# Optimization experiments

Hardware: AMD Instinct MI355X
Metric: run time of the kernel (lower is better)

## Reference

```python
import jax, jax.numpy as jnp
import numpy as np

N = 100000   # nodes
E = 220000   # directed edges (each branch)
H = 128      # hidden_dim
OUT = 1      # output_dim
G = 4096     # num graphs in batch
PE = 5       # laplacian eigenvector PE dims
VOCAB = 28   # atom types


def gcn_conv(x, src, dst, W, b, n):
    # PyG GCNConv: x' = D^-1/2 (A + I) D^-1/2 (X W) + b
    h = x @ W
    deg = jax.ops.segment_sum(jnp.ones(src.shape[0], x.dtype), dst, num_segments=n) + 1.0
    dinv = jax.lax.rsqrt(deg)
    coef = dinv[src] * dinv[dst]                                    # [E]
    agg = jax.ops.segment_sum(h[src] * coef[:, None], dst, num_segments=n)
    agg = agg + h * (dinv * dinv)[:, None]                          # self-loop term
    return agg + b


def gcn2(x, edge_index, W1, b1, W2, b2, n):
    # PyG GCN model, num_layers=2: conv -> relu -> conv
    src, dst = edge_index[0], edge_index[1]
    h = jax.nn.relu(gcn_conv(x, src, dst, W1, b1, n))
    return gcn_conv(h, src, dst, W2, b2, n)


def setup_inputs() -> dict:
    key = jax.random.key(0)
    ks = jax.random.split(key, 16)
    s = 0.1
    return {
        "node_tokens": jax.random.randint(ks[0], (N, 1), 0, VOCAB),
        "pe": jax.random.normal(ks[1], (N, PE), jnp.float32),
        "edge_index": jax.random.randint(ks[2], (2, E), 0, N),
        "vr_edge_index": jax.random.randint(ks[3], (2, E), 0, N),
        "batch": jnp.sort(jax.random.randint(ks[4], (N,), 0, G)),
        "embed_table": jax.random.normal(ks[5], (VOCAB, H), jnp.float32) * s,
        "Wt": jax.random.normal(ks[6], (PE, H), jnp.float32) * s,
        "bt": jnp.zeros((H,), jnp.float32),
        "W1": jax.random.normal(ks[7], (H, H), jnp.float32) * s,
        "b1": jnp.zeros((H,), jnp.float32),
        "W2": jax.random.normal(ks[8], (H, OUT), jnp.float32) * s,
        "b2": jnp.zeros((OUT,), jnp.float32),
        "Wv1": jax.random.normal(ks[9], (H, H), jnp.float32) * s,
        "bv1": jnp.zeros((H,), jnp.float32),
        "Wv2": jax.random.normal(ks[10], (H, OUT), jnp.float32) * s,
        "bv2": jnp.zeros((OUT,), jnp.float32),
    }


def reference(node_tokens, pe, edge_index, vr_edge_index, batch, embed_table,
              Wt, bt, W1, b1, W2, b2, Wv1, bv1, Wv2, bv2):
    # embed_x(data.x.long()).squeeze(1) + lin_trans(pe)
    x = embed_table[node_tokens[:, 0]] + (pe @ Wt + bt)             # [N, H]
    x1 = gcn2(x, edge_index, W1, b1, W2, b2, N)                     # [N, OUT]
    xv = gcn2(x, vr_edge_index, Wv1, bv1, Wv2, bv2, N)              # [N, OUT]
    x1 = x1 + xv
    y_hat = jax.ops.segment_sum(x1, batch, num_segments=G)          # [G, OUT]
    y_hat = jnp.squeeze(y_hat, axis=-1)                             # [G]
    return (y_hat, x)
```

## Files before the change

kernel.cpp:

```cpp
#include <hip/hip_runtime.h>

#define NN 100000
#define NE 220000
#define HD 128
#define NG 4096
#define NPE 5
#define NB_SCAN ((NN + 255) / 256)
#define NBX4 ((NN * HD / 4) / 256)
#define NBW 128
#define NBD ((2 * NE + 255) / 256)
#define NBAG ((NN + 63) / 64)
#define LDP 136

typedef unsigned int uint;
typedef unsigned short ushort;
typedef __attribute__((ext_vector_type(8))) short bf16x8;
typedef __attribute__((ext_vector_type(4))) float f32x4;

__device__ __forceinline__ float bf2f(uint u16) {
    return __uint_as_float(u16 << 16);
}
__device__ __forceinline__ ushort f2bf(float f) {
    uint u = __float_as_uint(f);
    u += 0x7fffu + ((u >> 16) & 1u);
    return (ushort)(u >> 16);
}

__global__ void k_front(const int* __restrict__ tok, const float* __restrict__ pe,
                        const float* __restrict__ embed, const float* __restrict__ Wtr,
                        const float* __restrict__ bt,
                        float* __restrict__ x, ushort* __restrict__ xb,
                        const float* __restrict__ W1, const float* __restrict__ Wv1,
                        ushort* __restrict__ Wcat,
                        const int* __restrict__ ei, const int* __restrict__ vei,
                        int* __restrict__ cnt) {
    int b = blockIdx.x;
    if (b < NBX4) {
        int idx = b * 256 + threadIdx.x;
        int n = idx >> 5, q = idx & 31;
        int t = tok[n];
        float4 acc = ((const float4*)(embed + (size_t)t * HD))[q];
        float4 bv = ((const float4*)bt)[q];
        acc.x += bv.x; acc.y += bv.y; acc.z += bv.z; acc.w += bv.w;
        const float* pen = pe + n * NPE;
#pragma unroll
        for (int k = 0; k < NPE; ++k) {
            float p = pen[k];
            float4 wv = ((const float4*)(Wtr + k * HD))[q];
            acc.x += p * wv.x; acc.y += p * wv.y;
            acc.z += p * wv.z; acc.w += p * wv.w;
        }
        ((float4*)x)[idx] = acc;
        uint2 pk;
        pk.x = (uint)f2bf(acc.x) | ((uint)f2bf(acc.y) << 16);
        pk.y = (uint)f2bf(acc.z) | ((uint)f2bf(acc.w) << 16);
        ((uint2*)xb)[idx] = pk;
    } else if (b < NBX4 + NBW) {
        int t = (b - NBX4) * 256 + threadIdx.x;
        int f = t >> 7, k = t & 127;
        const float* W = (f < HD) ? W1 : Wv1;
        Wcat[t] = f2bf(W[k * HD + (f & 127)]);
    } else {
        int t = (b - NBX4 - NBW) * 256 + threadIdx.x;
        if (t < 2 * NE) {
            int br = t >= NE;
            int e = t - br * NE;
            const int* S = br ? vei : ei;
            atomicAdd(&cnt[br * NN + S[NE + e]], 1);
        }
    }
}

__global__ void k_scan1(const int* __restrict__ cnt, int* __restrict__ off,
                        int* __restrict__ bsum, float* __restrict__ dinv) {
    __shared__ int s[256];
    int br = blockIdx.x / NB_SCAN;
    int blk = blockIdx.x % NB_SCAN;
    int tid = threadIdx.x;
    int i = blk * 256 + tid;
    int v = (i < NN) ? cnt[br * NN + i] : 0;
    if (i < NN) dinv[br * NN + i] = rsqrtf((float)v + 1.0f);
    s[tid] = v;
    __syncthreads();
    for (int d = 1; d < 256; d <<= 1) {
        int t = (tid >= d) ? s[tid - d] : 0;
        __syncthreads();
        s[tid] += t;
        __syncthreads();
    }
    if (i < NN) off[br * NN + i] = s[tid] - v;
    if (tid == 255) bsum[br * 512 + blk] = s[255];
}

__global__ void k_scan2(int* __restrict__ bsum) {
    __shared__ int s[512];
    int br = blockIdx.x;
    int tid = threadIdx.x;
    int v = (tid < NB_SCAN) ? bsum[br * 512 + tid] : 0;
    s[tid] = v;
    __syncthreads();
    for (int d = 1; d < 512; d <<= 1) {
        int t = (tid >= d) ? s[tid - d] : 0;
        __syncthreads();
        s[tid] += t;
        __syncthreads();
    }
    if (tid < NB_SCAN) bsum[br * 512 + tid] = s[tid] - v;
}

__global__ void k_scan3(int* __restrict__ off, const int* __restrict__ bsum,
                        int* __restrict__ cur) {
    int br = blockIdx.x / NB_SCAN;
    int blk = blockIdx.x % NB_SCAN;
    int i = blk * 256 + threadIdx.x;
    if (i < NN) {
        int o = off[br * NN + i] + bsum[br * 512 + blk];
        off[br * NN + i] = o;
        cur[br * NN + i] = o;
    }
}

__global__ void k_scatter(const int* __restrict__ ei, const int* __restrict__ vei,
                          const float* __restrict__ dinv, int* __restrict__ cur,
                          int2* __restrict__ ent) {
    int t = blockIdx.x * blockDim.x + threadIdx.x;
    if (t >= 2 * NE) return;
    int br = t >= NE;
    int e = t - br * NE;
    const int* S = br ? vei : ei;
    int s = S[e], d = S[NE + e];
    int pos = atomicAdd(&cur[br * NN + d], 1);
    int2 rec;
    rec.x = s;
    rec.y = __float_as_int(dinv[br * NN + s] * dinv[br * NN + d]);
    ent[br * NE + pos] = rec;
}

__global__ __launch_bounds__(256) void k_agg_gemm(
        const ushort* __restrict__ xb, const ushort* __restrict__ Wcat,
        const float* __restrict__ dinv, const int* __restrict__ off,
        const int* __restrict__ cur, const int2* __restrict__ ent,
        const float* __restrict__ b1, const float* __restrict__ bv1,
        const float* __restrict__ W2, const float* __restrict__ Wv2,
        float* __restrict__ z) {
    __shared__ ushort As[64 * LDP];
    int bi = blockIdx.x;
    int br = bi >= NBAG;
    int n0 = (bi - br * NBAG) * 64;
    int tid = threadIdx.x;

    {
        int hw = tid >> 5;
        int l = tid & 31;
        const int2* en = ent + br * NE;
        for (int nn = 0; nn < 8; ++nn) {
            int nl = hw * 8 + nn;
            int n = n0 + nl;
            uint2 pk = {0u, 0u};
            if (n < NN) {
                float dv = dinv[br * NN + n];
                uint2 u = *(const uint2*)(xb + (size_t)n * HD + l * 4);
                float c = dv * dv;
                float a0 = bf2f(u.x & 0xffffu) * c, a1 = bf2f(u.x >> 16) * c;
                float a2 = bf2f(u.y & 0xffffu) * c, a3 = bf2f(u.y >> 16) * c;
                int p0 = off[br * NN + n], p1 = cur[br * NN + n];
                for (int p = p0; p < p1; p += 4) {
                    int2 e0 = en[p], e1 = en[p + 1], e2 = en[p + 2], e3 = en[p + 3];
                    int s0 = e0.x;
                    int s1 = (p + 1 < p1) ? e1.x : n;
                    int s2 = (p + 2 < p1) ? e2.x : n;
                    int s3 = (p + 3 < p1) ? e3.x : n;
                    float c0 = __int_as_float(e0.y);
                    float c1 = (p + 1 < p1) ? __int_as_float(e1.y) : 0.f;
                    float c2 = (p + 2 < p1) ? __int_as_float(e2.y) : 0.f;
                    float c3 = (p + 3 < p1) ? __int_as_float(e3.y) : 0.f;
                    uint2 v0 = *(const uint2*)(xb + (size_t)s0 * HD + l * 4);
                    uint2 v1 = *(const uint2*)(xb + (size_t)s1 * HD + l * 4);
                    uint2 v2 = *(const uint2*)(xb + (size_t)s2 * HD + l * 4);
                    uint2 v3 = *(const uint2*)(xb + (size_t)s3 * HD + l * 4);
                    a0 += bf2f(v0.x & 0xffffu) * c0; a1 += bf2f(v0.x >> 16) * c0;
                    a2 += bf2f(v0.y & 0xffffu) * c0; a3 += bf2f(v0.y >> 16) * c0;
                    a0 += bf2f(v1.x & 0xffffu) * c1; a1 += bf2f(v1.x >> 16) * c1;
                    a2 += bf2f(v1.y & 0xffffu) * c1; a3 += bf2f(v1.y >> 16) * c1;
                    a0 += bf2f(v2.x & 0xffffu) * c2; a1 += bf2f(v2.x >> 16) * c2;
                    a2 += bf2f(v2.y & 0xffffu) * c2; a3 += bf2f(v2.y >> 16) * c2;
                    a0 += bf2f(v3.x & 0xffffu) * c3; a1 += bf2f(v3.x >> 16) * c3;
                    a2 += bf2f(v3.y & 0xffffu) * c3; a3 += bf2f(v3.y >> 16) * c3;
                }
                pk.x = (uint)f2bf(a0) | ((uint)f2bf(a1) << 16);
                pk.y = (uint)f2bf(a2) | ((uint)f2bf(a3) << 16);
            }
            *(uint2*)&As[nl * LDP + l * 4] = pk;
        }
    }
    __syncthreads();

    int w = tid >> 6, lane = tid & 63;
    int m = lane & 15, quad = lane >> 4;
    const ushort* Wg = Wcat + (size_t)br * 128 * 128;
    f32x4 acc[8] = {};
#pragma unroll
    for (int kc = 0; kc < 4; ++kc) {
        int k0 = kc * 32 + quad * 8;
        bf16x8 xf = *(const bf16x8*)&As[(w * 16 + m) * LDP + k0];
#pragma unroll
        for (int ft = 0; ft < 8; ++ft) {
            bf16x8 wf = *(const bf16x8*)&Wg[(ft * 16 + m) * 128 + k0];
            acc[ft] = __builtin_amdgcn_mfma_f32_16x16x32_bf16(wf, xf, acc[ft], 0, 0, 0);
        }
    }
    const float* bb = br ? bv1 : b1;
    const float* ww = br ? Wv2 : W2;
    float part = 0.f;
#pragma unroll
    for (int ft = 0; ft < 8; ++ft) {
        int f0 = ft * 16 + quad * 4;
        float4 b4 = *(const float4*)&bb[f0];
        float4 w4 = *(const float4*)&ww[f0];
        f32x4 a = acc[ft];
        part += fmaxf(a[0] + b4.x, 0.f) * w4.x + fmaxf(a[1] + b4.y, 0.f) * w4.y
              + fmaxf(a[2] + b4.z, 0.f) * w4.z + fmaxf(a[3] + b4.w, 0.f) * w4.w;
    }
    part += __shfl_xor(part, 16);
    part += __shfl_xor(part, 32);
    int n = n0 + w * 16 + m;
    if (quad == 0 && n < NN) z[br * NN + n] = part;
}

__global__ void k_final2(const float* __restrict__ z, const float* __restrict__ dinv,
                         const int* __restrict__ off, const int* __restrict__ cur,
                         const int2* __restrict__ ent,
                         const float* __restrict__ b2, const float* __restrict__ bv2,
                         const int* __restrict__ batch, float* __restrict__ y) {
    __shared__ float ybuf[256];
    __shared__ int gbase_s;
    int br = blockIdx.x >= NB_SCAN;
    int nb = blockIdx.x - br * NB_SCAN;
    int tid = threadIdx.x;
    ybuf[tid] = 0.f;
    if (tid == 0) gbase_s = batch[nb * 256];
    __syncthreads();
    int gbase = gbase_s;
    int n = nb * 256 + tid;
    if (n < NN) {
        const int2* en = ent + br * NE;
        float dv = dinv[br * NN + n];
        float acc = z[br * NN + n] * dv * dv;
        int p1 = cur[br * NN + n];
        for (int p = off[br * NN + n]; p < p1; p += 4) {
            int2 e0 = en[p], e1 = en[p + 1], e2 = en[p + 2], e3 = en[p + 3];
            int s0 = e0.x;
            int s1 = (p + 1 < p1) ? e1.x : n;
            int s2 = (p + 2 < p1) ? e2.x : n;
            int s3 = (p + 3 < p1) ? e3.x : n;
            float c0 = __int_as_float(e0.y);
            float c1 = (p + 1 < p1) ? __int_as_float(e1.y) : 0.f;
            float c2 = (p + 2 < p1) ? __int_as_float(e2.y) : 0.f;
            float c3 = (p + 3 < p1) ? __int_as_float(e3.y) : 0.f;
            acc += c0 * z[br * NN + s0] + c1 * z[br * NN + s1]
                 + c2 * z[br * NN + s2] + c3 * z[br * NN + s3];
        }
        acc += br ? bv2[0] : b2[0];
        int gi = batch[n] - gbase;
        if (gi < 256) atomicAdd(&ybuf[gi], acc);
        else atomicAdd(&y[batch[n]], acc);
    }
    __syncthreads();
    float v = ybuf[tid];
    if (v != 0.f) atomicAdd(&y[gbase + tid], v);
}

extern "C" void kernel_launch(void* const* d_in, const int* in_sizes, int n_in,
                              void* d_out, int out_size, void* d_ws, size_t ws_size,
                              hipStream_t stream) {
    const int*   tok   = (const int*)d_in[0];
    const float* pe    = (const float*)d_in[1];
    const int*   ei    = (const int*)d_in[2];
    const int*   vei   = (const int*)d_in[3];
    const int*   batch = (const int*)d_in[4];
    const float* embed = (const float*)d_in[5];
    const float* Wtr   = (const float*)d_in[6];
    const float* bt    = (const float*)d_in[7];
    const float* W1    = (const float*)d_in[8];
    const float* b1    = (const float*)d_in[9];
    const float* W2    = (const float*)d_in[10];
    const float* b2    = (const float*)d_in[11];
    const float* Wv1   = (const float*)d_in[12];
    const float* bv1   = (const float*)d_in[13];
    const float* Wv2   = (const float*)d_in[14];
    const float* bv2   = (const float*)d_in[15];

    float* y = (float*)d_out;
    float* x = y + NG;

    char* w = (char*)d_ws;
    ushort* xb   = (ushort*)w;               w += (size_t)NN * HD * 2;
    ushort* Wcat = (ushort*)w;               w += 256 * 128 * 2;
    float*  dinv = (float*)w;                w += 2 * NN * 4;
    float*  z    = (float*)w;                w += 2 * NN * 4;
    int*    cnt  = (int*)w;                  w += 2 * NN * 4;
    int*    off  = (int*)w;                  w += 2 * NN * 4;
    int*    cur  = (int*)w;                  w += 2 * NN * 4;
    int2*   ent  = (int2*)w;                 w += (size_t)(2 * NE + 8) * 8;
    int*    bsum = (int*)w;                  w += 2 * 512 * 4;

    hipMemsetAsync(y, 0, NG * sizeof(float), stream);
    hipMemsetAsync(cnt, 0, 2 * NN * sizeof(int), stream);

    k_front<<<NBX4 + NBW + NBD, 256, 0, stream>>>(tok, pe, embed, Wtr, bt, x, xb,
                                                  W1, Wv1, Wcat, ei, vei, cnt);
    k_scan1<<<2 * NB_SCAN, 256, 0, stream>>>(cnt, off, bsum, dinv);
    k_scan2<<<2, 512, 0, stream>>>(bsum);
    k_scan3<<<2 * NB_SCAN, 256, 0, stream>>>(off, bsum, cur);
    k_scatter<<<(2 * NE + 255) / 256, 256, 0, stream>>>(ei, vei, dinv, cur, ent);
    k_agg_gemm<<<2 * NBAG, 256, 0, stream>>>(xb, Wcat, dinv, off, cur, ent,
                                             b1, bv1, W2, Wv2, z);
    k_final2<<<2 * NB_SCAN, 256, 0, stream>>>(z, dinv, off, cur, ent,
                                              b2, bv2, batch, y);
}
```

Before: 274.6 us.

## Replace three-pass scan with atomic wave-level CSR allocation and shrink agg tiles

The three-kernel prefix scan becomes a single kernel in which each wavefront scans its counts with shuffles and reserves a contiguous range through an atomicAdd on a global allocator. This makes CSR segments non-ordered but still contiguous, and the zeroing of y moves into that kernel, removing two launches and a memset. The aggregation+GEMM kernel now handles 16 nodes per 512-thread block, one node per half-wave, instead of 64 nodes per 256 threads, to raise parallelism and cut per-thread serial gather work. The feature dimension is split across waves with a shared-memory reduction, at the cost of reloading W per block and adding a sync.

```diff
diff --git a/kernel.cpp b/kernel.cpp
--- a/kernel.cpp
+++ b/kernel.cpp
@@ -9,7 +9,7 @@
 #define NBX4 ((NN * HD / 4) / 256)
 #define NBW 128
 #define NBD ((2 * NE + 255) / 256)
-#define NBAG ((NN + 63) / 64)
+#define NBAG16 (NN / 16)
 #define LDP 136
 
 typedef unsigned int uint;
@@ -71,50 +71,32 @@
     }
 }
 
-__global__ void k_scan1(const int* __restrict__ cnt, int* __restrict__ off,
-                        int* __restrict__ bsum, float* __restrict__ dinv) {
-    __shared__ int s[256];
-    int br = blockIdx.x / NB_SCAN;
-    int blk = blockIdx.x % NB_SCAN;
+__global__ void k_alloc(const int* __restrict__ cnt, int* __restrict__ alloc,
+                        float* __restrict__ dinv, int* __restrict__ off,
+                        int* __restrict__ cur, float* __restrict__ y) {
     int tid = threadIdx.x;
+    int gid = blockIdx.x * 256 + tid;
+    if (gid < NG) y[gid] = 0.f;
+    int br = blockIdx.x >= NB_SCAN;
+    int blk = blockIdx.x - br * NB_SCAN;
     int i = blk * 256 + tid;
-    int v = (i < NN) ? cnt[br * NN + i] : 0;
-    if (i < NN) dinv[br * NN + i] = rsqrtf((float)v + 1.0f);
-    s[tid] = v;
-    __syncthreads();
-    for (int d = 1; d < 256; d <<= 1) {
-        int t = (tid >= d) ? s[tid - d] : 0;
-        __syncthreads();
-        s[tid] += t;
-        __syncthreads();
-    }
-    if (i < NN) off[br * NN + i] = s[tid] - v;
-    if (tid == 255) bsum[br * 512 + blk] = s[255];
-}
-
-__global__ void k_scan2(int* __restrict__ bsum) {
-    __shared__ int s[512];
-    int br = blockIdx.x;
-    int tid = threadIdx.x;
-    int v = (tid < NB_SCAN) ? bsum[br * 512 + tid] : 0;
-    s[tid] = v;
-    __syncthreads();
-    for (int d = 1; d < 512; d <<= 1) {
-        int t = (tid >= d) ? s[tid - d] : 0;
-        __syncthreads();
-        s[tid] += t;
-        __syncthreads();
-    }
-    if (tid < NB_SCAN) bsum[br * 512 + tid] = s[tid] - v;
-}
-
-__global__ void k_scan3(int* __restrict__ off, const int* __restrict__ bsum,
-                        int* __restrict__ cur) {
-    int br = blockIdx.x / NB_SCAN;
-    int blk = blockIdx.x % NB_SCAN;
-    int i = blk * 256 + threadIdx.x;
+    int lane = tid & 63;
+    int c = 0;
     if (i < NN) {
-        int o = off[br * NN + i] + bsum[br * 512 + blk];
+        c = cnt[br * NN + i];
+        dinv[br * NN + i] = rsqrtf((float)c + 1.0f);
+    }
+    int x = c;
+#pragma unroll
+    for (int o = 1; o < 64; o <<= 1) {
+        int t = __shfl_up(x, o, 64);
+        if (lane >= o) x += t;
+    }
+    int bs = 0;
+    if (lane == 63) bs = atomicAdd(&alloc[br], x);
+    bs = __shfl(bs, 63, 64);
+    if (i < NN) {
+        int o = bs + x - c;
         off[br * NN + i] = o;
         cur[br * NN + i] = o;
     }
@@ -136,95 +118,89 @@
     ent[br * NE + pos] = rec;
 }
 
-__global__ __launch_bounds__(256) void k_agg_gemm(
+__global__ __launch_bounds__(512) void k_agg_gemm(
         const ushort* __restrict__ xb, const ushort* __restrict__ Wcat,
         const float* __restrict__ dinv, const int* __restrict__ off,
         const int* __restrict__ cur, const int2* __restrict__ ent,
         const float* __restrict__ b1, const float* __restrict__ bv1,
         const float* __restrict__ W2, const float* __restrict__ Wv2,
         float* __restrict__ z) {
-    __shared__ ushort As[64 * LDP];
+    __shared__ ushort As[16 * LDP];
+    __shared__ float red[8][16];
     int bi = blockIdx.x;
-    int br = bi >= NBAG;
-    int n0 = (bi - br * NBAG) * 64;
+    int br = bi >= NBAG16;
+    int n0 = (bi - br * NBAG16) * 16;
     int tid = threadIdx.x;
 
     {
-        int hw = tid >> 5;
+        int h = tid >> 5;
         int l = tid & 31;
+        int n = n0 + h;
         const int2* en = ent + br * NE;
-        for (int nn = 0; nn < 8; ++nn) {
-            int nl = hw * 8 + nn;
-            int n = n0 + nl;
-            uint2 pk = {0u, 0u};
-            if (n < NN) {
-                float dv = dinv[br * NN + n];
-                uint2 u = *(const uint2*)(xb + (size_t)n * HD + l * 4);
-                float c = dv * dv;
-                float a0 = bf2f(u.x & 0xffffu) * c, a1 = bf2f(u.x >> 16) * c;
-                float a2 = bf2f(u.y & 0xffffu) * c, a3 = bf2f(u.y >> 16) * c;
-                int p0 = off[br * NN + n], p1 = cur[br * NN + n];
-                for (int p = p0; p < p1; p += 4) {
-                    int2 e0 = en[p], e1 = en[p + 1], e2 = en[p + 2], e3 = en[p + 3];
-                    int s0 = e0.x;
-                    int s1 = (p + 1 < p1) ? e1.x : n;
-                    int s2 = (p + 2 < p1) ? e2.x : n;
-                    int s3 = (p + 3 < p1) ? e3.x : n;
-                    float c0 = __int_as_float(e0.y);
-                    float c1 = (p + 1 < p1) ? __int_as_float(e1.y) : 0.f;
-                    float c2 = (p + 2 < p1) ? __int_as_float(e2.y) : 0.f;
-                    float c3 = (p + 3 < p1) ? __int_as_float(e3.y) : 0.f;
-                    uint2 v0 = *(const uint2*)(xb + (size_t)s0 * HD + l * 4);
-                    uint2 v1 = *(const uint2*)(xb + (size_t)s1 * HD + l * 4);
-                    uint2 v2 = *(const uint2*)(xb + (size_t)s2 * HD + l * 4);
-                    uint2 v3 = *(const uint2*)(xb + (size_t)s3 * HD + l * 4);
-                    a0 += bf2f(v0.x & 0xffffu) * c0; a1 += bf2f(v0.x >> 16) * c0;
-                    a2 += bf2f(v0.y & 0xffffu) * c0; a3 += bf2f(v0.y >> 16) * c0;
-                    a0 += bf2f(v1.x & 0xffffu) * c1; a1 += bf2f(v1.x >> 16) * c1;
-                    a2 += bf2f(v1.y & 0xffffu) * c1; a3 += bf2f(v1.y >> 16) * c1;
-                    a0 += bf2f(v2.x & 0xffffu) * c2; a1 += bf2f(v2.x >> 16) * c2;
-                    a2 += bf2f(v2.y & 0xffffu) * c2; a3 += bf2f(v2.y >> 16) * c2;
-                    a0 += bf2f(v3.x & 0xffffu) * c3; a1 += bf2f(v3.x >> 16) * c3;
-                    a2 += bf2f(v3.y & 0xffffu) * c3; a3 += bf2f(v3.y >> 16) * c3;
-                }
-                pk.x = (uint)f2bf(a0) | ((uint)f2bf(a1) << 16);
-                pk.y = (uint)f2bf(a2) | ((uint)f2bf(a3) << 16);
-            }
-            *(uint2*)&As[nl * LDP + l * 4] = pk;
-        }
+        float dv = dinv[br * NN + n];
+        uint2 u = *(const uint2*)(xb + (size_t)n * HD + l * 4);
+        float c = dv * dv;
+        float a0 = bf2f(u.x & 0xffffu) * c, a1 = bf2f(u.x >> 16) * c;
+        float a2 = bf2f(u.y & 0xffffu) * c, a3 = bf2f(u.y >> 16) * c;
+        int p0 = off[br * NN + n], p1 = cur[br * NN + n];
+        for (int p = p0; p < p1; p += 4) {
+            int2 e0 = en[p], e1 = en[p + 1], e2 = en[p + 2], e3 = en[p + 3];
+            int s0 = e0.x;
+            int s1 = (p + 1 < p1) ? e1.x : n;
+            int s2 = (p + 2 < p1) ? e2.x : n;
+            int s3 = (p + 3 < p1) ? e3.x : n;
+            float c0 = __int_as_float(e0.y);
+            float c1 = (p + 1 < p1) ? __int_as_float(e1.y) : 0.f;
+            float c2 = (p + 2 < p1) ? __int_as_float(e2.y) : 0.f;
+            float c3 = (p + 3 < p1) ? __int_as_float(e3.y) : 0.f;
+            uint2 v0 = *(const uint2*)(xb + (size_t)s0 * HD + l * 4);
+            uint2 v1 = *(const uint2*)(xb + (size_t)s1 * HD + l * 4);
+            uint2 v2 = *(const uint2*)(xb + (size_t)s2 * HD + l * 4);
+            uint2 v3 = *(const uint2*)(xb + (size_t)s3 * HD + l * 4);
+            a0 += bf2f(v0.x & 0xffffu) * c0; a1 += bf2f(v0.x >> 16) * c0;
+            a2 += bf2f(v0.y & 0xffffu) * c0; a3 += bf2f(v0.y >> 16) * c0;
+            a0 += bf2f(v1.x & 0xffffu) * c1; a1 += bf2f(v1.x >> 16) * c1;
+            a2 += bf2f(v1.y & 0xffffu) * c1; a3 += bf2f(v1.y >> 16) * c1;
+            a0 += bf2f(v2.x & 0xffffu) * c2; a1 += bf2f(v2.x >> 16) * c2;
+            a2 += bf2f(v2.y & 0xffffu) * c2; a3 += bf2f(v2.y >> 16) * c2;
+            a0 += bf2f(v3.x & 0xffffu) * c3; a1 += bf2f(v3.x >> 16) * c3;
+            a2 += bf2f(v3.y & 0xffffu) * c3; a3 += bf2f(v3.y >> 16) * c3;
+        }
+        uint2 pk;
+        pk.x = (uint)f2bf(a0) | ((uint)f2bf(a1) << 16);
+        pk.y = (uint)f2bf(a2) | ((uint)f2bf(a3) << 16);
+        *(uint2*)&As[h * LDP + l * 4] = pk;
     }
     __syncthreads();
 
     int w = tid >> 6, lane = tid & 63;
     int m = lane & 15, quad = lane >> 4;
     const ushort* Wg = Wcat + (size_t)br * 128 * 128;
-    f32x4 acc[8] = {};
+    f32x4 acc = {};
 #pragma unroll
     for (int kc = 0; kc < 4; ++kc) {
         int k0 = kc * 32 + quad * 8;
-        bf16x8 xf = *(const bf16x8*)&As[(w * 16 + m) * LDP + k0];
-#pragma unroll
-        for (int ft = 0; ft < 8; ++ft) {
-            bf16x8 wf = *(const bf16x8*)&Wg[(ft * 16 + m) * 128 + k0];
-            acc[ft] = __builtin_amdgcn_mfma_f32_16x16x32_bf16(wf, xf, acc[ft], 0, 0, 0);
-        }
+        bf16x8 xf = *(const bf16x8*)&As[m * LDP + k0];
+        bf16x8 wf = *(const bf16x8*)&Wg[(w * 16 + m) * 128 + k0];
+        acc = __builtin_amdgcn_mfma_f32_16x16x32_bf16(wf, xf, acc, 0, 0, 0);
     }
     const float* bb = br ? bv1 : b1;
     const float* ww = br ? Wv2 : W2;
-    float part = 0.f;
-#pragma unroll
-    for (int ft = 0; ft < 8; ++ft) {
-        int f0 = ft * 16 + quad * 4;
-        float4 b4 = *(const float4*)&bb[f0];
-        float4 w4 = *(const float4*)&ww[f0];
-        f32x4 a = acc[ft];
-        part += fmaxf(a[0] + b4.x, 0.f) * w4.x + fmaxf(a[1] + b4.y, 0.f) * w4.y
-              + fmaxf(a[2] + b4.z, 0.f) * w4.z + fmaxf(a[3] + b4.w, 0.f) * w4.w;
-    }
+    int f0 = w * 16 + quad * 4;
+    float4 b4 = *(const float4*)&bb[f0];
+    float4 w4 = *(const float4*)&ww[f0];
+    float part = fmaxf(acc[0] + b4.x, 0.f) * w4.x + fmaxf(acc[1] + b4.y, 0.f) * w4.y
+               + fmaxf(acc[2] + b4.z, 0.f) * w4.z + fmaxf(acc[3] + b4.w, 0.f) * w4.w;
     part += __shfl_xor(part, 16);
     part += __shfl_xor(part, 32);
-    int n = n0 + w * 16 + m;
-    if (quad == 0 && n < NN) z[br * NN + n] = part;
+    if (lane < 16) red[w][lane] = part;
+    __syncthreads();
+    if (tid < 16) {
+        float s = 0.f;
+#pragma unroll
+        for (int i = 0; i < 8; ++i) s += red[i][tid];
+        z[br * NN + n0 + tid] = s;
+    }
 }
 
 __global__ void k_final2(const float* __restrict__ z, const float* __restrict__ dinv,
@@ -298,23 +274,20 @@
     ushort* Wcat = (ushort*)w;               w += 256 * 128 * 2;
     float*  dinv = (float*)w;                w += 2 * NN * 4;
     float*  z    = (float*)w;                w += 2 * NN * 4;
-    int*    cnt  = (int*)w;                  w += 2 * NN * 4;
+    int*    cnt  = (int*)w;                  w += (2 * NN + 2) * 4;
     int*    off  = (int*)w;                  w += 2 * NN * 4;
     int*    cur  = (int*)w;                  w += 2 * NN * 4;
     int2*   ent  = (int2*)w;                 w += (size_t)(2 * NE + 8) * 8;
-    int*    bsum = (int*)w;                  w += 2 * 512 * 4;
-
-    hipMemsetAsync(y, 0, NG * sizeof(float), stream);
-    hipMemsetAsync(cnt, 0, 2 * NN * sizeof(int), stream);
+    int*    alloc = cnt + 2 * NN;
+
+    hipMemsetAsync(cnt, 0, (2 * NN + 2) * sizeof(int), stream);
 
     k_front<<<NBX4 + NBW + NBD, 256, 0, stream>>>(tok, pe, embed, Wtr, bt, x, xb,
                                                   W1, Wv1, Wcat, ei, vei, cnt);
-    k_scan1<<<2 * NB_SCAN, 256, 0, stream>>>(cnt, off, bsum, dinv);
-    k_scan2<<<2, 512, 0, stream>>>(bsum);
-    k_scan3<<<2 * NB_SCAN, 256, 0, stream>>>(off, bsum, cur);
+    k_alloc<<<2 * NB_SCAN, 256, 0, stream>>>(cnt, alloc, dinv, off, cur, y);
     k_scatter<<<(2 * NE + 255) / 256, 256, 0, stream>>>(ei, vei, dinv, cur, ent);
-    k_agg_gemm<<<2 * NBAG, 256, 0, stream>>>(xb, Wcat, dinv, off, cur, ent,
-                                             b1, bv1, W2, Wv2, z);
+    k_agg_gemm<<<2 * NBAG16, 512, 0, stream>>>(xb, Wcat, dinv, off, cur, ent,
+                                               b1, bv1, W2, Wv2, z);
     k_final2<<<2 * NB_SCAN, 256, 0, stream>>>(z, dinv, off, cur, ent,
                                               b2, bv2, batch, y);
 }
```

Result: slower. 289.0 us (+5.2%).

## Parallelize aggregation over edges with LDS fp32 atomics and 512-thread blocks

Applied to the files above, without the earlier changes.

The aggregation in the fused agg+GEMM kernel now distributes the edge range of each 64-node tile across 16 half-waves instead of assigning 8 nodes per half-wave. Partial sums accumulate in a swizzled fp32 LDS tile through shared-memory atomics, which requires storing the destination node in each CSR entry (int2 widened to int4). The GEMM is remapped so each of 8 waves owns 16 output features across all 64 nodes, followed by a cross-wave reduction. The y memset is folded into the scan kernel. This targets load imbalance from skewed degrees, at the cost of doubled entry bandwidth, LDS atomic contention and 32KB+ of LDS per block.

```diff
diff --git a/kernel.cpp b/kernel.cpp
--- a/kernel.cpp
+++ b/kernel.cpp
@@ -9,7 +9,7 @@
 #define NBX4 ((NN * HD / 4) / 256)
 #define NBW 128
 #define NBD ((2 * NE + 255) / 256)
-#define NBAG ((NN + 63) / 64)
+#define NBT ((NN + 63) / 64)
 #define LDP 136
 
 typedef unsigned int uint;
@@ -72,11 +72,14 @@
 }
 
 __global__ void k_scan1(const int* __restrict__ cnt, int* __restrict__ off,
-                        int* __restrict__ bsum, float* __restrict__ dinv) {
+                        int* __restrict__ bsum, float* __restrict__ dinv,
+                        float* __restrict__ y) {
     __shared__ int s[256];
+    int tid = threadIdx.x;
+    int gid = blockIdx.x * 256 + tid;
+    if (gid < NG) y[gid] = 0.f;
     int br = blockIdx.x / NB_SCAN;
     int blk = blockIdx.x % NB_SCAN;
-    int tid = threadIdx.x;
     int i = blk * 256 + tid;
     int v = (i < NN) ? cnt[br * NN + i] : 0;
     if (i < NN) dinv[br * NN + i] = rsqrtf((float)v + 1.0f);
@@ -122,7 +125,7 @@
 
 __global__ void k_scatter(const int* __restrict__ ei, const int* __restrict__ vei,
                           const float* __restrict__ dinv, int* __restrict__ cur,
-                          int2* __restrict__ ent) {
+                          int4* __restrict__ ent) {
     int t = blockIdx.x * blockDim.x + threadIdx.x;
     if (t >= 2 * NE) return;
     int br = t >= NE;
@@ -130,67 +133,69 @@
     const int* S = br ? vei : ei;
     int s = S[e], d = S[NE + e];
     int pos = atomicAdd(&cur[br * NN + d], 1);
-    int2 rec;
+    int4 rec;
     rec.x = s;
     rec.y = __float_as_int(dinv[br * NN + s] * dinv[br * NN + d]);
+    rec.z = d;
+    rec.w = 0;
     ent[br * NE + pos] = rec;
 }
 
-__global__ __launch_bounds__(256) void k_agg_gemm(
+__global__ __launch_bounds__(512) void k_agg_gemm(
         const ushort* __restrict__ xb, const ushort* __restrict__ Wcat,
         const float* __restrict__ dinv, const int* __restrict__ off,
-        const int* __restrict__ cur, const int2* __restrict__ ent,
+        const int4* __restrict__ ent,
         const float* __restrict__ b1, const float* __restrict__ bv1,
         const float* __restrict__ W2, const float* __restrict__ Wv2,
         float* __restrict__ z) {
-    __shared__ ushort As[64 * LDP];
+    __shared__ float acc[64 * 128];
+    __shared__ float red[8][64];
     int bi = blockIdx.x;
-    int br = bi >= NBAG;
-    int n0 = (bi - br * NBAG) * 64;
+    int br = bi >= NBT;
+    int n0 = (bi - br * NBT) * 64;
     int tid = threadIdx.x;
+    int hw = tid >> 5, l = tid & 31;
+
+#pragma unroll
+    for (int r = 0; r < 4; ++r) {
+        int nl = r * 16 + hw;
+        int n = n0 + nl;
+        float4 v = {0.f, 0.f, 0.f, 0.f};
+        if (n < NN) {
+            float dv = dinv[br * NN + n];
+            float c = dv * dv;
+            uint2 u = *(const uint2*)(xb + (size_t)n * HD + l * 4);
+            v.x = bf2f(u.x & 0xffffu) * c;
+            v.y = bf2f(u.x >> 16) * c;
+            v.z = bf2f(u.y & 0xffffu) * c;
+            v.w = bf2f(u.y >> 16) * c;
+        }
+        *(float4*)&acc[nl * 128 + ((l ^ (nl & 7)) << 2)] = v;
+    }
+    __syncthreads();
 
     {
-        int hw = tid >> 5;
-        int l = tid & 31;
-        const int2* en = ent + br * NE;
-        for (int nn = 0; nn < 8; ++nn) {
-            int nl = hw * 8 + nn;
-            int n = n0 + nl;
-            uint2 pk = {0u, 0u};
-            if (n < NN) {
-                float dv = dinv[br * NN + n];
-                uint2 u = *(const uint2*)(xb + (size_t)n * HD + l * 4);
-                float c = dv * dv;
-                float a0 = bf2f(u.x & 0xffffu) * c, a1 = bf2f(u.x >> 16) * c;
-                float a2 = bf2f(u.y & 0xffffu) * c, a3 = bf2f(u.y >> 16) * c;
-                int p0 = off[br * NN + n], p1 = cur[br * NN + n];
-                for (int p = p0; p < p1; p += 4) {
-                    int2 e0 = en[p], e1 = en[p + 1], e2 = en[p + 2], e3 = en[p + 3];
-                    int s0 = e0.x;
-                    int s1 = (p + 1 < p1) ? e1.x : n;
-                    int s2 = (p + 2 < p1) ? e2.x : n;
-                    int s3 = (p + 3 < p1) ? e3.x : n;
-                    float c0 = __int_as_float(e0.y);
-                    float c1 = (p + 1 < p1) ? __int_as_float(e1.y) : 0.f;
-                    float c2 = (p + 2 < p1) ? __int_as_float(e2.y) : 0.f;
-                    float c3 = (p + 3 < p1) ? __int_as_float(e3.y) : 0.f;
-                    uint2 v0 = *(const uint2*)(xb + (size_t)s0 * HD + l * 4);
-                    uint2 v1 = *(const uint2*)(xb + (size_t)s1 * HD + l * 4);
-                    uint2 v2 = *(const uint2*)(xb + (size_t)s2 * HD + l * 4);
-                    uint2 v3 = *(const uint2*)(xb + (size_t)s3 * HD + l * 4);
-                    a0 += bf2f(v0.x & 0xffffu) * c0; a1 += bf2f(v0.x >> 16) * c0;
-                    a2 += bf2f(v0.y & 0xffffu) * c0; a3 += bf2f(v0.y >> 16) * c0;
-                    a0 += bf2f(v1.x & 0xffffu) * c1; a1 += bf2f(v1.x >> 16) * c1;
-                    a2 += bf2f(v1.y & 0xffffu) * c1; a3 += bf2f(v1.y >> 16) * c1;
-                    a0 += bf2f(v2.x & 0xffffu) * c2; a1 += bf2f(v2.x >> 16) * c2;
-                    a2 += bf2f(v2.y & 0xffffu) * c2; a3 += bf2f(v2.y >> 16) * c2;
-                    a0 += bf2f(v3.x & 0xffffu) * c3; a1 += bf2f(v3.x >> 16) * c3;
-                    a2 += bf2f(v3.y & 0xffffu) * c3; a3 += bf2f(v3.y >> 16) * c3;
-                }
-                pk.x = (uint)f2bf(a0) | ((uint)f2bf(a1) << 16);
-                pk.y = (uint)f2bf(a2) | ((uint)f2bf(a3) << 16);
-            }
-            *(uint2*)&As[nl * LDP + l * 4] = pk;
+        int p0 = off[br * NN + n0];
+        int p1 = (n0 + 64 < NN) ? off[br * NN + n0 + 64] : NE;
+        const int4* E = ent + br * NE;
+        int p = p0 + hw;
+        int4 r0;
+        if (p < p1) r0 = E[p];
+        while (p < p1) {
+            int pn = p + 16;
+            int4 r1;
+            if (pn < p1) r1 = E[pn];
+            int src = r0.x;
+            float cf = __int_as_float(r0.y);
+            int nl = r0.z - n0;
+            uint2 v = *(const uint2*)(xb + (size_t)src * HD + l * 4);
+            float* a = &acc[nl * 128 + ((l ^ (nl & 7)) << 2)];
+            atomicAdd(a + 0, bf2f(v.x & 0xffffu) * cf);
+            atomicAdd(a + 1, bf2f(v.x >> 16) * cf);
+            atomicAdd(a + 2, bf2f(v.y & 0xffffu) * cf);
+            atomicAdd(a + 3, bf2f(v.y >> 16) * cf);
+            r0 = r1;
+            p = pn;
         }
     }
     __syncthreads();
@@ -198,38 +203,55 @@
     int w = tid >> 6, lane = tid & 63;
     int m = lane & 15, quad = lane >> 4;
     const ushort* Wg = Wcat + (size_t)br * 128 * 128;
-    f32x4 acc[8] = {};
+    f32x4 a4[4] = {};
 #pragma unroll
     for (int kc = 0; kc < 4; ++kc) {
         int k0 = kc * 32 + quad * 8;
-        bf16x8 xf = *(const bf16x8*)&As[(w * 16 + m) * LDP + k0];
-#pragma unroll
-        for (int ft = 0; ft < 8; ++ft) {
-            bf16x8 wf = *(const bf16x8*)&Wg[(ft * 16 + m) * 128 + k0];
-            acc[ft] = __builtin_amdgcn_mfma_f32_16x16x32_bf16(wf, xf, acc[ft], 0, 0, 0);
+        bf16x8 wf = *(const bf16x8*)&Wg[(w * 16 + m) * 128 + k0];
+        int c0 = k0 >> 2;
+#pragma unroll
+        for (int nt = 0; nt < 4; ++nt) {
+            int nl = nt * 16 + m;
+            const float* rowb = &acc[nl * 128];
+            float4 lo = *(const float4*)&rowb[((c0) ^ (nl & 7)) << 2];
+            float4 hi = *(const float4*)&rowb[((c0 + 1) ^ (nl & 7)) << 2];
+            bf16x8 xf;
+            xf[0] = (short)f2bf(lo.x); xf[1] = (short)f2bf(lo.y);
+            xf[2] = (short)f2bf(lo.z); xf[3] = (short)f2bf(lo.w);
+            xf[4] = (short)f2bf(hi.x); xf[5] = (short)f2bf(hi.y);
+            xf[6] = (short)f2bf(hi.z); xf[7] = (short)f2bf(hi.w);
+            a4[nt] = __builtin_amdgcn_mfma_f32_16x16x32_bf16(wf, xf, a4[nt], 0, 0, 0);
         }
     }
     const float* bb = br ? bv1 : b1;
     const float* ww = br ? Wv2 : W2;
-    float part = 0.f;
-#pragma unroll
-    for (int ft = 0; ft < 8; ++ft) {
-        int f0 = ft * 16 + quad * 4;
-        float4 b4 = *(const float4*)&bb[f0];
-        float4 w4 = *(const float4*)&ww[f0];
-        f32x4 a = acc[ft];
-        part += fmaxf(a[0] + b4.x, 0.f) * w4.x + fmaxf(a[1] + b4.y, 0.f) * w4.y
-              + fmaxf(a[2] + b4.z, 0.f) * w4.z + fmaxf(a[3] + b4.w, 0.f) * w4.w;
-    }
-    part += __shfl_xor(part, 16);
-    part += __shfl_xor(part, 32);
-    int n = n0 + w * 16 + m;
-    if (quad == 0 && n < NN) z[br * NN + n] = part;
+    int f0 = w * 16 + quad * 4;
+    float4 b4 = *(const float4*)&bb[f0];
+    float4 w4 = *(const float4*)&ww[f0];
+#pragma unroll
+    for (int nt = 0; nt < 4; ++nt) {
+        f32x4 a = a4[nt];
+        float part = fmaxf(a[0] + b4.x, 0.f) * w4.x + fmaxf(a[1] + b4.y, 0.f) * w4.y
+                   + fmaxf(a[2] + b4.z, 0.f) * w4.z + fmaxf(a[3] + b4.w, 0.f) * w4.w;
+        part += __shfl_xor(part, 16);
+        part += __shfl_xor(part, 32);
+        if (lane < 16) red[w][nt * 16 + lane] = part;
+    }
+    __syncthreads();
+    if (tid < 64) {
+        int n = n0 + tid;
+        if (n < NN) {
+            float s = 0.f;
+#pragma unroll
+            for (int i = 0; i < 8; ++i) s += red[i][tid];
+            z[br * NN + n] = s;
+        }
+    }
 }
 
 __global__ void k_final2(const float* __restrict__ z, const float* __restrict__ dinv,
                          const int* __restrict__ off, const int* __restrict__ cur,
-                         const int2* __restrict__ ent,
+                         const int4* __restrict__ ent,
                          const float* __restrict__ b2, const float* __restrict__ bv2,
                          const int* __restrict__ batch, float* __restrict__ y) {
     __shared__ float ybuf[256];
@@ -243,12 +265,12 @@
     int gbase = gbase_s;
     int n = nb * 256 + tid;
     if (n < NN) {
-        const int2* en = ent + br * NE;
+        const int4* en = ent + br * NE;
         float dv = dinv[br * NN + n];
         float acc = z[br * NN + n] * dv * dv;
         int p1 = cur[br * NN + n];
         for (int p = off[br * NN + n]; p < p1; p += 4) {
-            int2 e0 = en[p], e1 = en[p + 1], e2 = en[p + 2], e3 = en[p + 3];
+            int4 e0 = en[p], e1 = en[p + 1], e2 = en[p + 2], e3 = en[p + 3];
             int s0 = e0.x;
             int s1 = (p + 1 < p1) ? e1.x : n;
             int s2 = (p + 2 < p1) ? e2.x : n;
@@ -301,20 +323,19 @@
     int*    cnt  = (int*)w;                  w += 2 * NN * 4;
     int*    off  = (int*)w;                  w += 2 * NN * 4;
     int*    cur  = (int*)w;                  w += 2 * NN * 4;
-    int2*   ent  = (int2*)w;                 w += (size_t)(2 * NE + 8) * 8;
+    int4*   ent  = (int4*)w;                 w += (size_t)(2 * NE + 8) * 16;
     int*    bsum = (int*)w;                  w += 2 * 512 * 4;
 
-    hipMemsetAsync(y, 0, NG * sizeof(float), stream);
     hipMemsetAsync(cnt, 0, 2 * NN * sizeof(int), stream);
 
     k_front<<<NBX4 + NBW + NBD, 256, 0, stream>>>(tok, pe, embed, Wtr, bt, x, xb,
                                                   W1, Wv1, Wcat, ei, vei, cnt);
-    k_scan1<<<2 * NB_SCAN, 256, 0, stream>>>(cnt, off, bsum, dinv);
+    k_scan1<<<2 * NB_SCAN, 256, 0, stream>>>(cnt, off, bsum, dinv, y);
     k_scan2<<<2, 512, 0, stream>>>(bsum);
     k_scan3<<<2 * NB_SCAN, 256, 0, stream>>>(off, bsum, cur);
     k_scatter<<<(2 * NE + 255) / 256, 256, 0, stream>>>(ei, vei, dinv, cur, ent);
-    k_agg_gemm<<<2 * NBAG, 256, 0, stream>>>(xb, Wcat, dinv, off, cur, ent,
-                                             b1, bv1, W2, Wv2, z);
+    k_agg_gemm<<<2 * NBT, 512, 0, stream>>>(xb, Wcat, dinv, off, ent,
+                                            b1, bv1, W2, Wv2, z);
     k_final2<<<2 * NB_SCAN, 256, 0, stream>>>(z, dinv, off, cur, ent,
                                               b2, bv2, batch, y);
 }
```

Result: slower. 491.5 us (+79.0%).
